# Kernel tuning notes

Measured on AMD Instinct MI355X. Metric: run time of the kernel, lower is better.

The kernel has to match this reference:

```python
import jax, jax.numpy as jnp
import numpy as np

MAG = 1.0
TAU = 0.5
B, D, C = 8192, 256, 128


def setup_inputs() -> dict:
    key = jax.random.key(0)
    k1, k2 = jax.random.split(key)
    outputs = jax.random.normal(k1, (B, D), dtype=jnp.float32)
    labels = jax.random.normal(k2, (B, C), dtype=jnp.float32)
    return {"outputs": outputs, "labels": labels}


def reference(outputs, labels):
    # Cosine-similarity matrix of labels, min-max normalized to [0, 1]
    norm2labels = labels / (jnp.linalg.norm(labels, axis=1, keepdims=True) + 1e-12)
    sim_mat = norm2labels @ norm2labels.T  # [B, B]
    sim_mat = (sim_mat - sim_mat.min()) / (sim_mat.max() - sim_mat.min())

    # Pairwise Euclidean distances of outputs via the Gram trick
    # ||x_i - x_j||^2 = ||x_i||^2 + ||x_j||^2 - 2 <x_i, x_j>
    sq = jnp.sum(outputs * outputs, axis=1)  # [B]
    d2 = sq[:, None] + sq[None, :] - 2.0 * (outputs @ outputs.T)  # [B, B]
    d2 = jnp.maximum(d2, 0.0)
    nz = d2 > 0.0
    # safe sqrt: zero (diagonal) entries get distance 0 with zero gradient,
    # matching torch.norm's subgradient at 0
    eud = jnp.sqrt(jnp.where(nz, d2, 1.0)) * nz
    eud = eud / eud.max()

    distance = eud + sim_mat  # [B, B]
    pos_mask = sim_mat > TAU

    # Per-row masked log-sum-exp terms (distance in [0, 2], no overflow risk)
    pos_loss = jnp.log(jnp.sum(jnp.where(pos_mask, jnp.exp(distance), 0.0), axis=1))
    neg_loss = jnp.log(jnp.sum(jnp.where(pos_mask, 0.0, jnp.exp(MAG - distance)), axis=1))

    # clamp negatives (and -inf from empty masks) to 0, as the original `if < 0` does
    loss = jnp.maximum(pos_loss, 0.0) + jnp.maximum(neg_loss, 0.0)
    return jnp.mean(loss)
```

## Files before the change

### kernel.cpp

```cpp
#include <hip/hip_runtime.h>
#include <hip/hip_bf16.h>


#define B_N 8192
#define NT   64
#define TILE 128
#define NTRI 2080

typedef __attribute__((ext_vector_type(8))) short bf16x8;
typedef __attribute__((ext_vector_type(4))) float f32x4;
typedef __attribute__((ext_vector_type(2))) _Float16 f16x2;

__device__ __forceinline__ unsigned fenc(float f) {
    unsigned u = __float_as_uint(f);
    return (u & 0x80000000u) ? ~u : (u | 0x80000000u);
}
__device__ __forceinline__ float fdec(unsigned k) {
    unsigned u = (k & 0x80000000u) ? (k ^ 0x80000000u) : ~k;
    return __uint_as_float(u);
}
__device__ __forceinline__ unsigned pack2(float a, float b) {
    f16x2 p; p[0] = (_Float16)a; p[1] = (_Float16)b;
    return *(unsigned*)&p;
}

__device__ __forceinline__ void tile_decode(int b, int& bi, int& bj) {
    int si, sj, ti, tj;
    if (b < 544) {
        int sb = b / 136, w = b - sb * 136;
        int i = 0;
        while (w >= 16 - i) { w -= 16 - i; i++; }
        si = sb; sj = sb; ti = i; tj = i + w;
    } else {
        int q = (b - 544) >> 8, w = (b - 544) & 255;
        int i = 0;
        while (q >= 3 - i) { q -= 3 - i; i++; }
        si = i; sj = i + 1 + q;
        ti = w >> 4; tj = w & 15;
    }
    bi = si * 16 + ti; bj = sj * 16 + tj;
}

__global__ __launch_bounds__(256) void prep_kernel(
    const float* __restrict__ outputs, const float* __restrict__ labels,
    __hip_bfloat16* __restrict__ Obp, __hip_bfloat16* __restrict__ Lnp,
    float* __restrict__ sq, float* __restrict__ pos_sums,
    float* __restrict__ neg_sums, unsigned* __restrict__ stats) {
    int g = blockIdx.x, tid = threadIdx.x;
    int rl = tid >> 4, c = tid & 15;
    int row = g * 16 + rl;
    __shared__ __align__(16) short tO[16][264];
    __shared__ __align__(16) short tL[16][136];

    float s = 0.f;
    #pragma unroll
    for (int k = 0; k < 4; k++) {
        f32x4 v = *(const f32x4*)&outputs[(size_t)row * 256 + c * 16 + k * 4];
        s += v[0]*v[0] + v[1]*v[1] + v[2]*v[2] + v[3]*v[3];
        __hip_bfloat16 b4[4];
        #pragma unroll
        for (int i = 0; i < 4; i++) b4[i] = __float2bfloat16(v[i]);
        *(uint2*)&tO[rl][c * 16 + k * 4] = *(uint2*)b4;
    }
    #pragma unroll
    for (int m = 1; m < 16; m <<= 1) s += __shfl_xor(s, m);
    if (c == 0) sq[row] = s;

    float ls = 0.f;
    f32x4 u0 = *(const f32x4*)&labels[(size_t)row * 128 + c * 8];
    f32x4 u1 = *(const f32x4*)&labels[(size_t)row * 128 + c * 8 + 4];
    ls += u0[0]*u0[0] + u0[1]*u0[1] + u0[2]*u0[2] + u0[3]*u0[3];
    ls += u1[0]*u1[0] + u1[1]*u1[1] + u1[2]*u1[2] + u1[3]*u1[3];
    #pragma unroll
    for (int m = 1; m < 16; m <<= 1) ls += __shfl_xor(ls, m);
    float inv = 1.f / (sqrtf(ls) + 1e-12f);
    {
        __hip_bfloat16 b4[4];
        #pragma unroll
        for (int i = 0; i < 4; i++) b4[i] = __float2bfloat16(u0[i] * inv);
        *(uint2*)&tL[rl][c * 8] = *(uint2*)b4;
        #pragma unroll
        for (int i = 0; i < 4; i++) b4[i] = __float2bfloat16(u1[i] * inv);
        *(uint2*)&tL[rl][c * 8 + 4] = *(uint2*)b4;
    }
    if (tid < 16) { pos_sums[g * 16 + tid] = 0.f; neg_sums[g * 16 + tid] = 0.f; }
    if (g == 0 && tid == 0) {
        stats[0] = 0xFFFFFFFFu; stats[1] = 0u; stats[2] = 0u;
    }
    __syncthreads();

    #pragma unroll
    for (int q = 0; q < 2; q++) {
        int sl = tid * 2 + q;
        int o = sl >> 4, rr = sl & 15;
        uint4 d = *(uint4*)&tO[rr][o * 8];
        *(uint4*)&Obp[(size_t)g * 4096 + (size_t)sl * 8] = d;
    }
    {
        int o = tid >> 4, rr = tid & 15;
        uint4 d = *(uint4*)&tL[rr][o * 8];
        *(uint4*)&Lnp[(size_t)g * 2048 + (size_t)tid * 8] = d;
    }
}

template<int KD8>
__device__ __forceinline__ void gram_packed(
    const short* __restrict__ P, int rb16, int cb16, int lane,
    f32x4 (&acc)[4][4]) {
    #pragma unroll
    for (int mi = 0; mi < 4; mi++)
        #pragma unroll
        for (int ni = 0; ni < 4; ni++) {
            f32x4 z = {0.f, 0.f, 0.f, 0.f};
            acc[mi][ni] = z;
        }
    #pragma unroll
    for (int kc = 0; kc < KD8 / 4; kc++) {
        bf16x8 a[4], b[4];
        #pragma unroll
        for (int mi = 0; mi < 4; mi++)
            a[mi] = *(const bf16x8*)&P[((size_t)(rb16 + mi) * KD8 * 16
                                        + kc * 64 + lane) * 8];
        #pragma unroll
        for (int ni = 0; ni < 4; ni++)
            b[ni] = *(const bf16x8*)&P[((size_t)(cb16 + ni) * KD8 * 16
                                        + kc * 64 + lane) * 8];
        #pragma unroll
        for (int mi = 0; mi < 4; mi++)
            #pragma unroll
            for (int ni = 0; ni < 4; ni++)
                acc[mi][ni] = __builtin_amdgcn_mfma_f32_16x16x32_bf16(
                    a[mi], b[ni], acc[mi][ni], 0, 0, 0);
    }
}

__global__ __launch_bounds__(256, 3) void stats_kernel(
    const short* __restrict__ Lnp, const short* __restrict__ Obp,
    const float* __restrict__ sq, unsigned* __restrict__ stats) {
    int bi, bj;
    tile_decode(blockIdx.x, bi, bj);
    int tid = threadIdx.x, lane = tid & 63, wid = tid >> 6;
    int wm = (wid >> 1) * 64, wn = (wid & 1) * 64;
    int l15 = lane & 15, quad = lane >> 4;
    int rb16 = bi * 8 + (wid >> 1) * 4, cb16 = bj * 8 + (wid & 1) * 4;
    int rB = bi * TILE, cB = bj * TILE;

    float lmin = 1e30f, lmax = -1e30f, dmax = 0.f;
    f32x4 acc[4][4];

    gram_packed<16>(Lnp, rb16, cb16, lane, acc);
    #pragma unroll
    for (int mi = 0; mi < 4; mi++)
        #pragma unroll
        for (int ni = 0; ni < 4; ni++)
            #pragma unroll
            for (int r = 0; r < 4; r++) {
                float s = acc[mi][ni][r];
                lmin = fminf(lmin, s);
                lmax = fmaxf(lmax, s);
            }

    gram_packed<32>(Obp, rb16, cb16, lane, acc);
    float sqj[4];
    #pragma unroll
    for (int ni = 0; ni < 4; ni++) sqj[ni] = sq[cB + wn + ni * 16 + l15];
    #pragma unroll
    for (int mi = 0; mi < 4; mi++) {
        f32x4 sqi = *(const f32x4*)&sq[rB + wm + mi * 16 + quad * 4];
        #pragma unroll
        for (int r = 0; r < 4; r++)
            #pragma unroll
            for (int ni = 0; ni < 4; ni++) {
                float d2 = fmaxf(sqi[r] + sqj[ni] - 2.f * acc[mi][ni][r], 0.f);
                dmax = fmaxf(dmax, d2);
            }
    }

    #pragma unroll
    for (int m = 1; m < 64; m <<= 1) {
        lmin = fminf(lmin, __shfl_xor(lmin, m));
        lmax = fmaxf(lmax, __shfl_xor(lmax, m));
        dmax = fmaxf(dmax, __shfl_xor(dmax, m));
    }
    __shared__ float red[3][4];
    if ((tid & 63) == 0) { red[0][wid] = lmin; red[1][wid] = lmax; red[2][wid] = dmax; }
    __syncthreads();
    if (tid == 0) {
        lmin = fminf(fminf(red[0][0], red[0][1]), fminf(red[0][2], red[0][3]));
        lmax = fmaxf(fmaxf(red[1][0], red[1][1]), fmaxf(red[1][2], red[1][3]));
        dmax = fmaxf(fmaxf(red[2][0], red[2][1]), fmaxf(red[2][2], red[2][3]));
        atomicMin(&stats[0], fenc(lmin));
        atomicMax(&stats[1], fenc(lmax));
        atomicMax(&stats[2], fenc(dmax));
    }
}

__global__ __launch_bounds__(256, 3) void loss_kernel(
    const short* __restrict__ Lnp, const short* __restrict__ Obp,
    const float* __restrict__ sq, const unsigned* __restrict__ stats,
    float* __restrict__ pos_sums, float* __restrict__ neg_sums) {
    int bi, bj;
    tile_decode(blockIdx.x, bi, bj);
    int tid = threadIdx.x, lane = tid & 63, wid = tid >> 6;
    int wm = (wid >> 1) * 64, wn = (wid & 1) * 64;
    int l15 = lane & 15, quad = lane >> 4;
    int rb16 = bi * 8 + (wid >> 1) * 4, cb16 = bj * 8 + (wid & 1) * 4;
    int rB = bi * TILE, cB = bj * TILE;

    __shared__ unsigned simW[256 * 18];
    __shared__ float rP[TILE][2], rN[TILE][2];
    __shared__ float cP[TILE][2], cN[TILE][2];
    unsigned* my = &simW[tid * 18];

    f32x4 acc[4][4];

    gram_packed<16>(Lnp, rb16, cb16, lane, acc);
    #pragma unroll
    for (int mi = 0; mi < 4; mi++)
        #pragma unroll
        for (int ni = 0; ni < 4; ni++) {
            my[(mi * 4 + ni) * 2 + 0] = pack2(acc[mi][ni][0], acc[mi][ni][1]);
            my[(mi * 4 + ni) * 2 + 1] = pack2(acc[mi][ni][2], acc[mi][ni][3]);
        }

    gram_packed<32>(Obp, rb16, cb16, lane, acc);

    float smin = fdec(stats[0]);
    float smax = fdec(stats[1]);
    float d2max = fdec(stats[2]);
    float invr = 1.f / (smax - smin);
    float invem = rsqrtf(d2max);

    float sqj[4];
    #pragma unroll
    for (int ni = 0; ni < 4; ni++) sqj[ni] = sq[cB + wn + ni * 16 + l15];
    float cpsum[4] = {0.f, 0.f, 0.f, 0.f};
    float cnsum[4] = {0.f, 0.f, 0.f, 0.f};

    #pragma unroll
    for (int mi = 0; mi < 4; mi++) {
        f32x4 sqi = *(const f32x4*)&sq[rB + wm + mi * 16 + quad * 4];
        float ps[4] = {0.f, 0.f, 0.f, 0.f};
        float ns[4] = {0.f, 0.f, 0.f, 0.f};
        #pragma unroll
        for (int ni = 0; ni < 4; ni++) {
            f16x2 s01 = ((const f16x2*)my)[(mi * 4 + ni) * 2 + 0];
            f16x2 s23 = ((const f16x2*)my)[(mi * 4 + ni) * 2 + 1];
            #pragma unroll
            for (int r = 0; r < 4; r++) {
                float sraw = (r < 2) ? (float)s01[r] : (float)s23[r - 2];
                float sn = (sraw - smin) * invr;
                float g = acc[mi][ni][r];
                float d2 = fmaxf(sqi[r] + sqj[ni] - 2.f * g, 0.f);
                float eud = (d2 > 0.f) ? sqrtf(d2) * invem : 0.f;
                float dist = eud + sn;
                bool pos = sn > 0.5f;
                float pv = pos ? __expf(dist) : 0.f;
                float nv = pos ? 0.f : __expf(1.0f - dist);
                ps[r] += pv;  ns[r] += nv;
                cpsum[ni] += pv;  cnsum[ni] += nv;
            }
        }
        #pragma unroll
        for (int r = 0; r < 4; r++) {
            #pragma unroll
            for (int m = 1; m < 16; m <<= 1) {
                ps[r] += __shfl_xor(ps[r], m);
                ns[r] += __shfl_xor(ns[r], m);
            }
            if (l15 == 0) {
                int rr = wm + mi * 16 + quad * 4 + r;
                rP[rr][wid & 1] = ps[r];
                rN[rr][wid & 1] = ns[r];
            }
        }
    }
    #pragma unroll
    for (int ni = 0; ni < 4; ni++) {
        #pragma unroll
        for (int m = 16; m < 64; m <<= 1) {
            cpsum[ni] += __shfl_xor(cpsum[ni], m);
            cnsum[ni] += __shfl_xor(cnsum[ni], m);
        }
        if (quad == 0) {
            int cc = wn + ni * 16 + l15;
            cP[cc][wid >> 1] = cpsum[ni];
            cN[cc][wid >> 1] = cnsum[ni];
        }
    }
    __syncthreads();
    if (tid < TILE) {
        atomicAdd(&pos_sums[bi * TILE + tid], rP[tid][0] + rP[tid][1]);
        atomicAdd(&neg_sums[bi * TILE + tid], rN[tid][0] + rN[tid][1]);
        if (bi != bj) {
            atomicAdd(&pos_sums[bj * TILE + tid], cP[tid][0] + cP[tid][1]);
            atomicAdd(&neg_sums[bj * TILE + tid], cN[tid][0] + cN[tid][1]);
        }
    }
}

__global__ __launch_bounds__(256) void finalize_kernel(
    const float* __restrict__ pos_sums, const float* __restrict__ neg_sums,
    float* __restrict__ out) {
    int t = threadIdx.x;
    float acc = 0.f;
    for (int i = t; i < B_N; i += 256) {
        float p = pos_sums[i], n = neg_sums[i];
        float pl = fmaxf(logf(p), 0.f);
        float nl = (n > 0.f) ? fmaxf(logf(n), 0.f) : 0.f;
        acc += pl + nl;
    }
    #pragma unroll
    for (int m = 1; m < 64; m <<= 1) acc += __shfl_xor(acc, m);
    __shared__ float w4[4];
    if ((t & 63) == 0) w4[t >> 6] = acc;
    __syncthreads();
    if (t == 0) out[0] = (w4[0] + w4[1] + w4[2] + w4[3]) / (float)B_N;
}

extern "C" void kernel_launch(void* const* d_in, const int* in_sizes, int n_in,
                              void* d_out, int out_size, void* d_ws, size_t ws_size,
                              hipStream_t stream) {
    const float* outputs = (const float*)d_in[0];
    const float* labels  = (const float*)d_in[1];
    float* out = (float*)d_out;
    char* ws = (char*)d_ws;
    __hip_bfloat16* Obp = (__hip_bfloat16*)(ws);
    __hip_bfloat16* Lnp = (__hip_bfloat16*)(ws + 4194304);
    float* sq           = (float*)(ws + 6291456);
    float* pos_sums     = (float*)(ws + 6324224);
    float* neg_sums     = (float*)(ws + 6356992);
    unsigned* stats     = (unsigned*)(ws + 6389760);

    prep_kernel<<<B_N / 16, 256, 0, stream>>>(outputs, labels, Obp, Lnp, sq,
                                              pos_sums, neg_sums, stats);
    stats_kernel<<<NTRI, 256, 0, stream>>>((const short*)Lnp, (const short*)Obp,
                                           sq, stats);
    loss_kernel<<<NTRI, 256, 0, stream>>>((const short*)Lnp, (const short*)Obp,
                                          sq, stats, pos_sums, neg_sums);
    finalize_kernel<<<1, 256, 0, stream>>>(pos_sums, neg_sums, out);
}
```

Baseline: 222.4 us.

## Stage Gram operand tiles through LDS via global_load_lds instead of direct global loads

Both the stats and loss kernels now copy K-slices of the packed row and column operand blocks into shared memory with asynchronous global-to-LDS loads, then feed the MFMAs from LDS. Before, each wave read its fragments straight from global memory, so the same data was fetched by several waves. Sharing the fragments through LDS removes that redundant global traffic. In exchange it adds two barriers per slice with no double buffering, a larger LDS footprint, and occupancy lowered from 3 to 2 blocks per CU. The simW stride also changes from 18 to 33, apparently to avoid bank conflicts.

```diff
diff --git a/kernel.cpp b/kernel.cpp
--- a/kernel.cpp
+++ b/kernel.cpp
@@ -10,6 +10,9 @@
 typedef __attribute__((ext_vector_type(8))) short bf16x8;
 typedef __attribute__((ext_vector_type(4))) float f32x4;
 typedef __attribute__((ext_vector_type(2))) _Float16 f16x2;
+
+typedef const __attribute__((address_space(1))) void g_void;
+typedef __attribute__((address_space(3))) void l_void;
 
 __device__ __forceinline__ unsigned fenc(float f) {
     unsigned u = __float_as_uint(f);
@@ -104,9 +107,42 @@
 }
 
 template<int KD8>
-__device__ __forceinline__ void gram_packed(
-    const short* __restrict__ P, int rb16, int cb16, int lane,
-    f32x4 (&acc)[4][4]) {
+__device__ __forceinline__ void stage_slice(
+    const short* __restrict__ P, int g0, int o0, short* L, int tid) {
+    #pragma unroll
+    for (int p = 0; p < 4; p++) {
+        int u = p * 256 + tid;
+        int gl = u >> 7, off = u & 127;
+        size_t gu = ((size_t)(g0 + gl) * KD8 + o0) * 16 + off;
+        __builtin_amdgcn_global_load_lds((g_void*)(P + gu * 8),
+                                         (l_void*)(L + (size_t)u * 8), 16, 0, 0);
+    }
+}
+
+__device__ __forceinline__ void mfma_slice(
+    const short* As, const short* Bs, int wm4, int wn4,
+    int l15, int quad, f32x4 (&acc)[4][4]) {
+    #pragma unroll
+    for (int kc = 0; kc < 2; kc++) {
+        bf16x8 a[4], b[4];
+        #pragma unroll
+        for (int mi = 0; mi < 4; mi++)
+            a[mi] = *(const bf16x8*)&As[((wm4 + mi) * 128
+                                         + (kc * 4 + quad) * 16 + l15) * 8];
+        #pragma unroll
+        for (int ni = 0; ni < 4; ni++)
+            b[ni] = *(const bf16x8*)&Bs[((wn4 + ni) * 128
+                                         + (kc * 4 + quad) * 16 + l15) * 8];
+        #pragma unroll
+        for (int mi = 0; mi < 4; mi++)
+            #pragma unroll
+            for (int ni = 0; ni < 4; ni++)
+                acc[mi][ni] = __builtin_amdgcn_mfma_f32_16x16x32_bf16(
+                    a[mi], b[ni], acc[mi][ni], 0, 0, 0);
+    }
+}
+
+__device__ __forceinline__ void zero_acc(f32x4 (&acc)[4][4]) {
     #pragma unroll
     for (int mi = 0; mi < 4; mi++)
         #pragma unroll
@@ -114,41 +150,42 @@
             f32x4 z = {0.f, 0.f, 0.f, 0.f};
             acc[mi][ni] = z;
         }
-    #pragma unroll
-    for (int kc = 0; kc < KD8 / 4; kc++) {
-        bf16x8 a[4], b[4];
-        #pragma unroll
-        for (int mi = 0; mi < 4; mi++)
-            a[mi] = *(const bf16x8*)&P[((size_t)(rb16 + mi) * KD8 * 16
-                                        + kc * 64 + lane) * 8];
-        #pragma unroll
-        for (int ni = 0; ni < 4; ni++)
-            b[ni] = *(const bf16x8*)&P[((size_t)(cb16 + ni) * KD8 * 16
-                                        + kc * 64 + lane) * 8];
-        #pragma unroll
-        for (int mi = 0; mi < 4; mi++)
-            #pragma unroll
-            for (int ni = 0; ni < 4; ni++)
-                acc[mi][ni] = __builtin_amdgcn_mfma_f32_16x16x32_bf16(
-                    a[mi], b[ni], acc[mi][ni], 0, 0, 0);
-    }
-}
-
-__global__ __launch_bounds__(256, 3) void stats_kernel(
+}
+
+template<int KD8, int NS>
+__device__ __forceinline__ void gram_staged(
+    const short* __restrict__ P, int gA0, int gB0,
+    short* As, short* Bs, int tid, int wm4, int wn4,
+    int l15, int quad, f32x4 (&acc)[4][4]) {
+    #pragma unroll
+    for (int s = 0; s < NS; s++) {
+        __syncthreads();
+        stage_slice<KD8>(P, gA0, s * 8, As, tid);
+        stage_slice<KD8>(P, gB0, s * 8, Bs, tid);
+        __syncthreads();
+        mfma_slice(As, Bs, wm4, wn4, l15, quad, acc);
+    }
+}
+
+__global__ __launch_bounds__(256, 2) void stats_kernel(
     const short* __restrict__ Lnp, const short* __restrict__ Obp,
     const float* __restrict__ sq, unsigned* __restrict__ stats) {
     int bi, bj;
     tile_decode(blockIdx.x, bi, bj);
     int tid = threadIdx.x, lane = tid & 63, wid = tid >> 6;
     int wm = (wid >> 1) * 64, wn = (wid & 1) * 64;
+    int wm4 = (wid >> 1) * 4, wn4 = (wid & 1) * 4;
     int l15 = lane & 15, quad = lane >> 4;
-    int rb16 = bi * 8 + (wid >> 1) * 4, cb16 = bj * 8 + (wid & 1) * 4;
     int rB = bi * TILE, cB = bj * TILE;
+
+    __shared__ __align__(16) short As[1024 * 8];
+    __shared__ __align__(16) short Bs[1024 * 8];
 
     float lmin = 1e30f, lmax = -1e30f, dmax = 0.f;
     f32x4 acc[4][4];
 
-    gram_packed<16>(Lnp, rb16, cb16, lane, acc);
+    zero_acc(acc);
+    gram_staged<16, 2>(Lnp, bi * 8, bj * 8, As, Bs, tid, wm4, wn4, l15, quad, acc);
     #pragma unroll
     for (int mi = 0; mi < 4; mi++)
         #pragma unroll
@@ -160,7 +197,8 @@
                 lmax = fmaxf(lmax, s);
             }
 
-    gram_packed<32>(Obp, rb16, cb16, lane, acc);
+    zero_acc(acc);
+    gram_staged<32, 4>(Obp, bi * 8, bj * 8, As, Bs, tid, wm4, wn4, l15, quad, acc);
     float sqj[4];
     #pragma unroll
     for (int ni = 0; ni < 4; ni++) sqj[ni] = sq[cB + wn + ni * 16 + l15];
@@ -195,7 +233,7 @@
     }
 }
 
-__global__ __launch_bounds__(256, 3) void loss_kernel(
+__global__ __launch_bounds__(256, 2) void loss_kernel(
     const short* __restrict__ Lnp, const short* __restrict__ Obp,
     const float* __restrict__ sq, const unsigned* __restrict__ stats,
     float* __restrict__ pos_sums, float* __restrict__ neg_sums) {
@@ -203,18 +241,21 @@
     tile_decode(blockIdx.x, bi, bj);
     int tid = threadIdx.x, lane = tid & 63, wid = tid >> 6;
     int wm = (wid >> 1) * 64, wn = (wid & 1) * 64;
+    int wm4 = (wid >> 1) * 4, wn4 = (wid & 1) * 4;
     int l15 = lane & 15, quad = lane >> 4;
-    int rb16 = bi * 8 + (wid >> 1) * 4, cb16 = bj * 8 + (wid & 1) * 4;
     int rB = bi * TILE, cB = bj * TILE;
 
-    __shared__ unsigned simW[256 * 18];
+    __shared__ __align__(16) short As[1024 * 8];
+    __shared__ __align__(16) short Bs[1024 * 8];
+    __shared__ unsigned simW[256 * 33];
     __shared__ float rP[TILE][2], rN[TILE][2];
     __shared__ float cP[TILE][2], cN[TILE][2];
-    unsigned* my = &simW[tid * 18];
+    unsigned* my = &simW[tid * 33];
 
     f32x4 acc[4][4];
 
-    gram_packed<16>(Lnp, rb16, cb16, lane, acc);
+    zero_acc(acc);
+    gram_staged<16, 2>(Lnp, bi * 8, bj * 8, As, Bs, tid, wm4, wn4, l15, quad, acc);
     #pragma unroll
     for (int mi = 0; mi < 4; mi++)
         #pragma unroll
@@ -223,7 +264,8 @@
             my[(mi * 4 + ni) * 2 + 1] = pack2(acc[mi][ni][2], acc[mi][ni][3]);
         }
 
-    gram_packed<32>(Obp, rb16, cb16, lane, acc);
+    zero_acc(acc);
+    gram_staged<32, 4>(Obp, bi * 8, bj * 8, As, Bs, tid, wm4, wn4, l15, quad, acc);
 
     float smin = fdec(stats[0]);
     float smax = fdec(stats[1]);
```

After: 241.3 us. 8.5% more time.
